# Kernel optimization log

Measured on AMD Instinct MI355X. Metric: run time of the kernel, lower is better.

The kernel has to match this reference:

```python
import jax, jax.numpy as jnp
import numpy as np
from jax import lax
import math

B, T, CIN, H, W = 8, 64, 2, 64, 64
HID, SPK_C = 32, 64
D_MODEL, N_LAYERS, D_STATE, D_CONV = 512, 4, 16, 4
D_INNER = 2 * D_MODEL
DT_RANK = math.ceil(D_MODEL / 16)  # 32
NUM_CLASSES = 11
FEAT = SPK_C * (H // 4) * (W // 4)  # 16384
BETA, THR = 0.9, 1.0

# --- surrogate-gradient spike (snntorch fast_sigmoid, slope=25) ---
@jax.custom_vjp
def spike_fn(x):
    return (x > 0).astype(x.dtype)

def _spike_fwd(x):
    return spike_fn(x), x

def _spike_bwd(x, g):
    return (g / (25.0 * jnp.abs(x) + 1.0) ** 2,)

spike_fn.defvjp(_spike_fwd, _spike_bwd)

def lif(cur, mem):
    # snntorch Leaky, reset_mechanism='subtract': reset from previous mem (detached)
    reset = lax.stop_gradient((mem > THR).astype(mem.dtype))
    mem = BETA * mem + cur - reset * THR
    spk = spike_fn(mem - THR)
    return spk, mem

def conv2d(x, w, b):
    y = lax.conv_general_dilated(x, w, (1, 1), 'SAME', dimension_numbers=('NCHW', 'OIHW', 'NCHW'))
    return y + b[None, :, None, None]

def maxpool2(x):
    return lax.reduce_window(x, -jnp.inf, lax.max, (1, 1, 2, 2), (1, 1, 2, 2), 'VALID')

def layernorm(x, w, b):
    mu = x.mean(-1, keepdims=True)
    var = ((x - mu) ** 2).mean(-1, keepdims=True)
    return (x - mu) * lax.rsqrt(var + 1e-5) * w + b

def frontend(x, c1w, c1b, c2w, c2b, c3w, c3b):
    mem1 = jnp.zeros((B, HID, H // 2, W // 2), x.dtype)
    mem2 = jnp.zeros((B, HID, H // 4, W // 4), x.dtype)
    mem3 = jnp.zeros((B, SPK_C, H // 4, W // 4), x.dtype)
    def step(carry, xt):
        m1, m2, m3 = carry
        s1, m1 = lif(maxpool2(conv2d(xt, c1w, c1b)), m1)
        s2, m2 = lif(maxpool2(conv2d(s1, c2w, c2b)), m2)
        s3, m3 = lif(conv2d(s2, c3w, c3b), m3)
        return (m1, m2, m3), s3
    _, spk = lax.scan(step, (mem1, mem2, mem3), jnp.swapaxes(x, 0, 1))
    return jnp.swapaxes(spk, 0, 1)  # (B,T,SPK_C,H/4,W/4)

def rate_smooth(a):
    # depthwise conv1d over time with kernel ones(5)/5, padding=2 (moving average)
    Tn = a.shape[1]
    ap = jnp.pad(a, ((0, 0), (2, 2), (0, 0)))
    return sum(ap[:, k:k + Tn, :] for k in range(5)) / 5.0

def mamba_block(x, p):
    ln_w, ln_b, in_w, conv_w, xproj_w, dt_w, dt_b, A_log, Dp, out_w = p
    h = layernorm(x, ln_w, ln_b)
    xr = h @ in_w  # (B,L,2*D_INNER)
    xi, res = jnp.split(xr, 2, axis=-1)
    L = xi.shape[1]
    # causal depthwise conv1d (pad D_CONV-1 left, truncate to L)
    xp = jnp.pad(xi, ((0, 0), (D_CONV - 1, 0), (0, 0)))
    xc = sum(conv_w[:, k] * xp[:, k:k + L, :] for k in range(D_CONV))
    xc = jax.nn.silu(xc)
    x_dbl = xc @ xproj_w  # (B,L,DT_RANK+2*D_STATE)
    dt = x_dbl[..., :DT_RANK]
    Bm = x_dbl[..., DT_RANK:DT_RANK + D_STATE]
    Cm = x_dbl[..., DT_RANK + D_STATE:]
    dt = jax.nn.softplus(dt @ dt_w + dt_b)  # (B,L,D_INNER)
    A = -jnp.exp(A_log)  # (D_INNER,D_STATE)
    dA = jnp.exp(dt[..., None] * A)  # (B,L,D_INNER,D_STATE)
    dBu = dt[..., None] * Bm[:, :, None, :] * xc[..., None]
    def step(hst, inp):
        dA_t, dBu_t, C_t = inp
        hst = dA_t * hst + dBu_t
        return hst, jnp.einsum('bdn,bn->bd', hst, C_t)
    h0 = jnp.zeros((x.shape[0], D_INNER, D_STATE), x.dtype)
    _, ys = lax.scan(step, h0, (jnp.swapaxes(dA, 0, 1), jnp.swapaxes(dBu, 0, 1), jnp.swapaxes(Cm, 0, 1)))
    y = jnp.swapaxes(ys, 0, 1) + xc * Dp
    y = y * jax.nn.silu(res)
    return x + y @ out_w

def _forward(x, c1w, c1b, c2w, c2b, c3w, c3b, inp_w, inp_b, ln_w, ln_b, in_w, conv_w, xproj_w, dt_w, dt_b, A_log, Dp, mb_out_w, fn_w, fn_b, cls_w, cls_b):
    spikes = frontend(x, c1w, c1b, c2w, c2b, c3w, c3b)
    act = rate_smooth(spikes.reshape(B, T, -1))
    h = act @ inp_w + inp_b
    def layer(c, p):
        return mamba_block(c, p), None
    h, _ = lax.scan(layer, h, (ln_w, ln_b, in_w, conv_w, xproj_w, dt_w, dt_b, A_log, Dp, mb_out_w))
    h = h.mean(axis=1)
    h = layernorm(h, fn_w, fn_b)
    return h @ cls_w + cls_b

def setup_inputs():
    key = jax.random.key(0)
    ks = jax.random.split(key, 16)
    def gn(k, shape, scale):
        return jax.random.normal(k, shape, jnp.float32) * scale
    x = jax.random.uniform(ks[0], (B, T, CIN, H, W), jnp.float32)
    c1w = gn(ks[1], (HID, CIN, 3, 3), 1.0 / np.sqrt(CIN * 9)); c1b = jnp.zeros((HID,))
    c2w = gn(ks[2], (HID, HID, 3, 3), 1.0 / np.sqrt(HID * 9)); c2b = jnp.zeros((HID,))
    c3w = gn(ks[3], (SPK_C, HID, 3, 3), 1.0 / np.sqrt(HID * 9)); c3b = jnp.zeros((SPK_C,))
    inp_w = gn(ks[4], (FEAT, D_MODEL), 1.0 / np.sqrt(FEAT)); inp_b = jnp.zeros((D_MODEL,))
    ln_w = jnp.ones((N_LAYERS, D_MODEL)); ln_b = jnp.zeros((N_LAYERS, D_MODEL))
    in_w = gn(ks[5], (N_LAYERS, D_MODEL, 2 * D_INNER), 1.0 / np.sqrt(D_MODEL))
    conv_w = gn(ks[6], (N_LAYERS, D_INNER, D_CONV), 1.0 / np.sqrt(D_CONV))
    xproj_w = gn(ks[7], (N_LAYERS, D_INNER, DT_RANK + 2 * D_STATE), 1.0 / np.sqrt(D_INNER))
    dt_w = gn(ks[8], (N_LAYERS, DT_RANK, D_INNER), 1.0 / np.sqrt(DT_RANK))
    dtv = jnp.exp(jax.random.uniform(ks[9], (N_LAYERS, D_INNER)) * (np.log(0.1) - np.log(0.001)) + np.log(0.001))
    dt_b = dtv + jnp.log(-jnp.expm1(-dtv))
    A_log = jnp.log(jnp.broadcast_to(jnp.arange(1, D_STATE + 1, dtype=jnp.float32), (N_LAYERS, D_INNER, D_STATE))) + jnp.zeros((N_LAYERS, D_INNER, D_STATE))
    Dp = jnp.ones((N_LAYERS, D_INNER))
    mb_out_w = gn(ks[10], (N_LAYERS, D_INNER, D_MODEL), 1.0 / np.sqrt(D_INNER))
    fn_w = jnp.ones((D_MODEL,)); fn_b = jnp.zeros((D_MODEL,))
    cls_w = gn(ks[11], (D_MODEL, NUM_CLASSES), 1.0 / np.sqrt(D_MODEL)); cls_b = jnp.zeros((NUM_CLASSES,))
    return dict(x=x, c1w=c1w, c1b=c1b, c2w=c2w, c2b=c2b, c3w=c3w, c3b=c3b, inp_w=inp_w, inp_b=inp_b, ln_w=ln_w, ln_b=ln_b, in_w=in_w, conv_w=conv_w, xproj_w=xproj_w, dt_w=dt_w, dt_b=dt_b, A_log=A_log, Dp=Dp, mb_out_w=mb_out_w, fn_w=fn_w, fn_b=fn_b, cls_w=cls_w, cls_b=cls_b)

def reference(x, c1w, c1b, c2w, c2b, c3w, c3b, inp_w, inp_b, ln_w, ln_b, in_w, conv_w, xproj_w, dt_w, dt_b, A_log, Dp, mb_out_w, fn_w, fn_b, cls_w, cls_b):
    return _forward(x, c1w, c1b, c2w, c2b, c3w, c3b, inp_w, inp_b, ln_w, ln_b, in_w, conv_w, xproj_w, dt_w, dt_b, A_log, Dp, mb_out_w, fn_w, fn_b, cls_w, cls_b)
```

## Files before the change

kernel.cpp:

```cpp
#include <hip/hip_runtime.h>
#include <math.h>


static constexpr int TT = 64;
static constexpr float BETA = 0.9f, THR = 1.0f;


__global__ __launch_bounds__(256) void k_conv1pool(const float* __restrict__ x,
    const float* __restrict__ w, const float* __restrict__ bias, float* __restrict__ out)
{
    __shared__ float sI[2 * 66 * 76];
    __shared__ float sW[576];
    const int bt = blockIdx.x;
    const int tid = threadIdx.x;
    for (int i = tid; i < 2 * 66 * 76; i += 256) sI[i] = 0.f;
    for (int i = tid; i < 576; i += 256) sW[i] = w[i];
    __syncthreads();
    const float* img = x + (size_t)bt * 8192;
    for (int i = tid; i < 2048; i += 256) {
        float4 v4 = ((const float4*)img)[i];
        int lin = i * 4;
        int ci = lin >> 12, rc = lin & 4095;
        int r = rc >> 6, c = rc & 63;
        *(float4*)&sI[ci * 5016 + (r + 1) * 76 + (c + 4)] = v4;
    }
    __syncthreads();
    const int oh = tid >> 3;
    const int p8 = (tid & 7) * 8;
    float v[2][4][10];
    #pragma unroll
    for (int ci = 0; ci < 2; ++ci) {
        #pragma unroll
        for (int dr = 0; dr < 4; ++dr) {
            const float* rp = &sI[ci * 5016 + (2 * oh + dr) * 76 + p8];
            float2 a  = *(const float2*)&rp[2];
            float4 b4 = *(const float4*)&rp[4];
            float4 c4 = *(const float4*)&rp[8];
            float2 e  = *(const float2*)&rp[12];
            v[ci][dr][0] = a.y;
            v[ci][dr][1] = b4.x; v[ci][dr][2] = b4.y; v[ci][dr][3] = b4.z; v[ci][dr][4] = b4.w;
            v[ci][dr][5] = c4.x; v[ci][dr][6] = c4.y; v[ci][dr][7] = c4.z; v[ci][dr][8] = c4.w;
            v[ci][dr][9] = e.x;
        }
    }
    const int ow0 = (tid & 7) * 4;
    float* obase = out + (size_t)bt * 32768;
    for (int co = 0; co < 32; ++co) {
        float pos[2][8];
        #pragma unroll
        for (int i = 0; i < 2; ++i)
            #pragma unroll
            for (int j = 0; j < 8; ++j) pos[i][j] = 0.f;
        #pragma unroll
        for (int ci = 0; ci < 2; ++ci) {
            const float* wp = &sW[(co * 2 + ci) * 9];
            float w0=wp[0],w1=wp[1],w2=wp[2],w3=wp[3],w4=wp[4],w5=wp[5],w6=wp[6],w7=wp[7],w8=wp[8];
            #pragma unroll
            for (int pr = 0; pr < 2; ++pr)
                #pragma unroll
                for (int pc = 0; pc < 8; ++pc)
                    pos[pr][pc] += v[ci][pr][pc]*w0 + v[ci][pr][pc+1]*w1 + v[ci][pr][pc+2]*w2
                                 + v[ci][pr+1][pc]*w3 + v[ci][pr+1][pc+1]*w4 + v[ci][pr+1][pc+2]*w5
                                 + v[ci][pr+2][pc]*w6 + v[ci][pr+2][pc+1]*w7 + v[ci][pr+2][pc+2]*w8;
        }
        float b0 = bias[co];
        float4 o;
        o.x = fmaxf(fmaxf(pos[0][0], pos[0][1]), fmaxf(pos[1][0], pos[1][1])) + b0;
        o.y = fmaxf(fmaxf(pos[0][2], pos[0][3]), fmaxf(pos[1][2], pos[1][3])) + b0;
        o.z = fmaxf(fmaxf(pos[0][4], pos[0][5]), fmaxf(pos[1][4], pos[1][5])) + b0;
        o.w = fmaxf(fmaxf(pos[0][6], pos[0][7]), fmaxf(pos[1][6], pos[1][7])) + b0;
        *(float4*)&obase[co * 1024 + oh * 32 + ow0] = o;
    }
}

__global__ __launch_bounds__(256) void k_lif(const float* __restrict__ cur,
                                             float* __restrict__ spk, int chw)
{
    int idx = blockIdx.x * 256 + threadIdx.x;
    int b = idx / chw, p = idx % chw;
    const float* cp = cur + (size_t)b * TT * chw + p;
    float* sp = spk + (size_t)b * TT * chw + p;
    float m = 0.f;
    for (int t = 0; t < TT; ++t) {
        float c = cp[(size_t)t * chw];
        float reset = (m > THR) ? THR : 0.f;
        m = BETA * m + c - reset;
        sp[(size_t)t * chw] = (m > THR) ? 1.f : 0.f;
    }
}

__global__ __launch_bounds__(256) void k_conv2(const float* __restrict__ s1,
    const float* __restrict__ w, const float* __restrict__ bias, float* __restrict__ out)
{
    __shared__ float sI[4 * 34 * 40];
    __shared__ float sW2[4 * 8 * 12];
    const int bt = blockIdx.x;
    const int co0 = blockIdx.y * 8;
    const int tid = threadIdx.x;
    for (int i = tid; i < 4 * 34 * 40; i += 256) sI[i] = 0.f;
    const int cc = tid & 31;
    const int g8 = ((tid >> 5) & 3) * 8;
    const int cq = (tid >> 7) * 4;
    float acc[4][8] = {};
    const float* img = s1 + (size_t)bt * 32768;
    for (int chunk = 0; chunk < 8; ++chunk) {
        __syncthreads();
        const float* src = img + chunk * 4096;
        for (int i = tid; i < 1024; i += 256) {
            float4 v4 = ((const float4*)src)[i];
            int lin = i * 4;
            int ci = lin >> 10, rc = lin & 1023;
            int r = rc >> 5, c = rc & 31;
            *(float4*)&sI[ci * 1360 + (r + 1) * 40 + (c + 4)] = v4;
        }
        for (int i = tid; i < 4 * 8 * 9; i += 256) {
            int ci4 = i / 72, rest = i % 72;
            int co = rest / 9, k = rest % 9;
            sW2[(ci4 * 8 + co) * 12 + k] = w[((co0 + co) * 32 + chunk * 4 + ci4) * 9 + k];
        }
        __syncthreads();
        #pragma unroll
        for (int ci4 = 0; ci4 < 4; ++ci4) {
            float win[10][3];
            #pragma unroll
            for (int dr = 0; dr < 10; ++dr) {
                const float* sp = &sI[ci4 * 1360 + (g8 + dr) * 40 + cc + 3];
                win[dr][0] = sp[0]; win[dr][1] = sp[1]; win[dr][2] = sp[2];
            }
            #pragma unroll
            for (int co = 0; co < 4; ++co) {
                const float4* wq = (const float4*)&sW2[(ci4 * 8 + cq + co) * 12];
                float4 wa = wq[0], wb = wq[1], wc = wq[2];
                #pragma unroll
                for (int p = 0; p < 8; ++p)
                    acc[co][p] += win[p][0]*wa.x + win[p][1]*wa.y + win[p][2]*wa.z
                                + win[p+1][0]*wa.w + win[p+1][1]*wb.x + win[p+1][2]*wb.y
                                + win[p+2][0]*wb.z + win[p+2][1]*wb.w + win[p+2][2]*wc.x;
            }
        }
    }
    const bool writer = (cc & 1) == 0;
    #pragma unroll
    for (int co = 0; co < 4; ++co) {
        float b0 = bias[co0 + cq + co];
        float* ob = out + (size_t)bt * 8192 + (co0 + cq + co) * 256;
        #pragma unroll
        for (int i = 0; i < 4; ++i) {
            float v = fmaxf(acc[co][2 * i], acc[co][2 * i + 1]);
            v = fmaxf(v, __shfl_xor(v, 1, 64));
            if (writer) ob[(g8 / 2 + i) * 16 + (cc >> 1)] = v + b0;
        }
    }
}

__global__ __launch_bounds__(256) void k_conv3(const float* __restrict__ s2,
    const float* __restrict__ w, const float* __restrict__ bias, float* __restrict__ out)
{
    __shared__ float sI[8 * 18 * 24];
    __shared__ float sW3[8 * 32 * 12];
    const int bt = blockIdx.x;
    const int co0 = blockIdx.y * 32;
    const int tid = threadIdx.x;
    for (int i = tid; i < 8 * 18 * 24; i += 256) sI[i] = 0.f;
    const int cc = tid & 15;
    const int g8 = ((tid >> 4) & 1) * 8;
    const int cq = (tid >> 5) * 4;
    float acc[4][8] = {};
    const float* img = s2 + (size_t)bt * 8192;
    for (int chunk = 0; chunk < 4; ++chunk) {
        __syncthreads();
        const float* src = img + chunk * 2048;
        for (int i = tid; i < 512; i += 256) {
            float4 v4 = ((const float4*)src)[i];
            int lin = i * 4;
            int ci = lin >> 8, rc = lin & 255;
            int r = rc >> 4, c = rc & 15;
            *(float4*)&sI[ci * 432 + (r + 1) * 24 + (c + 4)] = v4;
        }
        for (int i = tid; i < 8 * 32 * 9; i += 256) {
            int ci = i / 288, rest = i % 288;
            int co = rest / 9, k = rest % 9;
            sW3[(ci * 32 + co) * 12 + k] = w[((co0 + co) * 32 + chunk * 8 + ci) * 9 + k];
        }
        __syncthreads();
        #pragma unroll
        for (int ci = 0; ci < 8; ++ci) {
            float win[10][3];
            #pragma unroll
            for (int dr = 0; dr < 10; ++dr) {
                const float* sp = &sI[ci * 432 + (g8 + dr) * 24 + cc + 3];
                win[dr][0] = sp[0]; win[dr][1] = sp[1]; win[dr][2] = sp[2];
            }
            #pragma unroll
            for (int co = 0; co < 4; ++co) {
                const float4* wq = (const float4*)&sW3[(ci * 32 + cq + co) * 12];
                float4 wa = wq[0], wb = wq[1], wc = wq[2];
                #pragma unroll
                for (int p = 0; p < 8; ++p)
                    acc[co][p] += win[p][0]*wa.x + win[p][1]*wa.y + win[p][2]*wa.z
                                + win[p+1][0]*wa.w + win[p+1][1]*wb.x + win[p+1][2]*wb.y
                                + win[p+2][0]*wb.z + win[p+2][1]*wb.w + win[p+2][2]*wc.x;
            }
        }
    }
    #pragma unroll
    for (int co = 0; co < 4; ++co) {
        float b0 = bias[co0 + cq + co];
        float* ob = out + (size_t)bt * 16384 + (co0 + cq + co) * 256;
        #pragma unroll
        for (int p = 0; p < 8; ++p)
            ob[(g8 + p) * 16 + cc] = acc[co][p] + b0;
    }
}

__global__ __launch_bounds__(256) void k_lif3smooth(const float* __restrict__ cur,
                                                    float* __restrict__ act)
{
    int idx = blockIdx.x * 256 + threadIdx.x;
    int b = idx >> 14, f = idx & 16383;
    const float* cp = cur + (size_t)b * TT * 16384 + f;
    float* ap = act + (size_t)b * TT * 16384 + f;
    float m = 0.f;
    float s0 = 0, s1 = 0, s2 = 0, s3 = 0, s4 = 0;
    for (int t = 0; t < TT + 2; ++t) {
        float s = 0.f;
        if (t < TT) {
            float cv = cp[(size_t)t * 16384];
            float reset = (m > THR) ? THR : 0.f;
            m = BETA * m + cv - reset;
            s = (m > THR) ? 1.f : 0.f;
        }
        s4 = s3; s3 = s2; s2 = s1; s1 = s0; s0 = s;
        if (t >= 2) ap[(size_t)(t - 2) * 16384] = (s0 + s1 + s2 + s3 + s4) * 0.2f;
    }
}


__global__ __launch_bounds__(256) void k_gemm(const float* __restrict__ A,
    const float* __restrict__ Bm, float* __restrict__ C, int M, int N, int K)
{
    __shared__ float As[16][68];
    __shared__ float Bs[16][68];
    const int tid = threadIdx.x;
    const int n0 = blockIdx.x * 64, m0 = blockIdx.y * 64;
    const int kchunk = K / gridDim.z;
    const int k0 = blockIdx.z * kchunk, k1 = k0 + kchunk;
    const int ar = tid >> 2, ac = (tid & 3) * 4;
    const int br = tid >> 4, bc = (tid & 15) * 4;
    const int row0 = (tid >> 4) * 4, col0 = (tid & 15) * 4;
    float acc[4][4] = {};
    float4 av = *(const float4*)&A[(size_t)(m0 + ar) * K + k0 + ac];
    float4 bv = *(const float4*)&Bm[(size_t)(k0 + br) * N + n0 + bc];
    for (int kk = k0; kk < k1; kk += 16) {
        As[ac + 0][ar] = av.x; As[ac + 1][ar] = av.y;
        As[ac + 2][ar] = av.z; As[ac + 3][ar] = av.w;
        *(float4*)&Bs[br][bc] = bv;
        __syncthreads();
        if (kk + 16 < k1) {
            av = *(const float4*)&A[(size_t)(m0 + ar) * K + kk + 16 + ac];
            bv = *(const float4*)&Bm[(size_t)(kk + 16 + br) * N + n0 + bc];
        }
        #pragma unroll
        for (int k = 0; k < 16; ++k) {
            float4 a4 = *(const float4*)&As[k][row0];
            float4 b4 = *(const float4*)&Bs[k][col0];
            acc[0][0] += a4.x * b4.x; acc[0][1] += a4.x * b4.y; acc[0][2] += a4.x * b4.z; acc[0][3] += a4.x * b4.w;
            acc[1][0] += a4.y * b4.x; acc[1][1] += a4.y * b4.y; acc[1][2] += a4.y * b4.z; acc[1][3] += a4.y * b4.w;
            acc[2][0] += a4.z * b4.x; acc[2][1] += a4.z * b4.y; acc[2][2] += a4.z * b4.z; acc[2][3] += a4.z * b4.w;
            acc[3][0] += a4.w * b4.x; acc[3][1] += a4.w * b4.y; acc[3][2] += a4.w * b4.z; acc[3][3] += a4.w * b4.w;
        }
        __syncthreads();
    }
    float* Cp = C + (size_t)blockIdx.z * M * N;
    #pragma unroll
    for (int i = 0; i < 4; ++i) {
        float4 o;
        o.x = acc[i][0]; o.y = acc[i][1]; o.z = acc[i][2]; o.w = acc[i][3];
        *(float4*)&Cp[(size_t)(m0 + row0 + i) * N + n0 + col0] = o;
    }
}

template <bool ADD, bool BIAS>
__global__ __launch_bounds__(256) void k_reduce(const float* __restrict__ part,
    const float* __restrict__ bias, float* __restrict__ out, int MN, int N, int KS)
{
    int i4 = (blockIdx.x * 256 + threadIdx.x) * 4;
    if (i4 >= MN) return;
    float4 v = {0.f, 0.f, 0.f, 0.f};
    for (int z = 0; z < KS; ++z) {
        float4 p = *(const float4*)&part[(size_t)z * MN + i4];
        v.x += p.x; v.y += p.y; v.z += p.z; v.w += p.w;
    }
    if (BIAS) {
        float4 bv = *(const float4*)&bias[i4 % N];
        v.x += bv.x; v.y += bv.y; v.z += bv.z; v.w += bv.w;
    }
    if (ADD) {
        float4 o = *(const float4*)&out[i4];
        v.x += o.x; v.y += o.y; v.z += o.z; v.w += o.w;
    }
    *(float4*)&out[i4] = v;
}


__device__ __forceinline__ float blockSum(float v, float* red)
{
    #pragma unroll
    for (int o = 32; o; o >>= 1) v += __shfl_down(v, o, 64);
    const int wv = threadIdx.x >> 6, lane = threadIdx.x & 63;
    if (lane == 0) red[wv] = v;
    __syncthreads();
    float r = red[0] + red[1] + red[2] + red[3];
    __syncthreads();
    return r;
}

__global__ __launch_bounds__(256) void k_ln(const float* __restrict__ x,
    const float* __restrict__ w, const float* __restrict__ b, float* __restrict__ out)
{
    __shared__ float red[4];
    int row = blockIdx.x;
    const float* xp = x + (size_t)row * 512;
    int c = threadIdx.x * 2;
    float2 v = *(const float2*)&xp[c];
    float mu = blockSum(v.x + v.y, red) * (1.f / 512.f);
    float d0 = v.x - mu, d1 = v.y - mu;
    float var = blockSum(d0 * d0 + d1 * d1, red) * (1.f / 512.f);
    float inv = rsqrtf(var + 1e-5f);
    float2 o;
    o.x = d0 * inv * w[c] + b[c];
    o.y = d1 * inv * w[c + 1] + b[c + 1];
    *(float2*)&out[(size_t)row * 512 + c] = o;
}

__global__ __launch_bounds__(256) void k_convsilu(const float* __restrict__ xr,
    const float* __restrict__ cw, float* __restrict__ xc)
{
    int idx = blockIdx.x * 256 + threadIdx.x;
    int row = idx >> 10;
    int d = idx & 1023;
    int t = row & 63;
    const float* xi = xr + (size_t)(row - t) * 2048 + d;
    float4 w = *(const float4*)&cw[d * 4];
    float a = w.w * xi[(size_t)t * 2048];
    if (t >= 1) a += w.z * xi[(size_t)(t - 1) * 2048];
    if (t >= 2) a += w.y * xi[(size_t)(t - 2) * 2048];
    if (t >= 3) a += w.x * xi[(size_t)(t - 3) * 2048];
    xc[idx] = a / (1.f + __expf(-a));
}

__global__ __launch_bounds__(256) void k_xproj(const float* __restrict__ xc,
    const float* __restrict__ w, float* __restrict__ xdbl)
{
    int row = blockIdx.x * 4 + (threadIdx.x >> 6);
    int col = threadIdx.x & 63;
    const float* a = xc + (size_t)row * 1024;
    float acc = 0.f;
    #pragma unroll 4
    for (int k = 0; k < 1024; k += 4) {
        float4 av = *(const float4*)&a[k];
        acc += av.x * w[(size_t)k * 64 + col] + av.y * w[(size_t)(k + 1) * 64 + col]
             + av.z * w[(size_t)(k + 2) * 64 + col] + av.w * w[(size_t)(k + 3) * 64 + col];
    }
    xdbl[(size_t)row * 64 + col] = acc;
}

__global__ __launch_bounds__(256) void k_dtproj(const float* __restrict__ xdbl,
    const float* __restrict__ w, const float* __restrict__ bias, float* __restrict__ dt)
{
    int idx = blockIdx.x * 256 + threadIdx.x;
    int row = idx >> 10, d = idx & 1023;
    const float* a = xdbl + (size_t)row * 64;
    float acc = bias[d];
    #pragma unroll 8
    for (int r = 0; r < 32; ++r) acc += a[r] * w[(size_t)r * 1024 + d];
    dt[idx] = fmaxf(acc, 0.f) + log1pf(__expf(-fabsf(acc)));
}

__global__ __launch_bounds__(256) void k_scan(const float* __restrict__ dt,
    const float* __restrict__ xc, const float* __restrict__ xdbl,
    const float* __restrict__ xr, const float* __restrict__ A_log,
    const float* __restrict__ Dp, float* __restrict__ y)
{
    const int tid = threadIdx.x;
    const int lane = tid & 63;
    const int half = lane >> 5;
    const int p = blockIdx.x * 128 + (tid >> 6) * 32 + (lane & 31);
    const int b = p >> 10, d = p & 1023;
    float A[8];
    #pragma unroll
    for (int n = 0; n < 8; ++n) A[n] = -__expf(A_log[d * 16 + half * 8 + n]);
    float Dv = Dp[d];
    float h[8] = {};
    const int row0 = b * 64;
    size_t base = (size_t)row0 * 1024 + d;
    float dtv = dt[base], xv = xc[base];
    float res = xr[(size_t)row0 * 2048 + 1024 + d];
    const float4* Bp = (const float4*)&xdbl[(size_t)row0 * 64 + 32 + half * 8];
    const float4* Cq = (const float4*)&xdbl[(size_t)row0 * 64 + 48 + half * 8];
    float4 B0 = Bp[0], B1 = Bp[1];
    float4 C0 = Cq[0], C1 = Cq[1];
    for (int t = 0; t < TT; ++t) {
        float dtv_n = 0.f, xv_n = 0.f, res_n = 0.f;
        float4 B0n = {}, B1n = {}, C0n = {}, C1n = {};
        if (t < TT - 1) {
            size_t b2 = base + (size_t)(t + 1) * 1024;
            dtv_n = dt[b2]; xv_n = xc[b2];
            res_n = xr[(size_t)(row0 + t + 1) * 2048 + 1024 + d];
            const float4* Bp2 = (const float4*)&xdbl[(size_t)(row0 + t + 1) * 64 + 32 + half * 8];
            const float4* Cq2 = (const float4*)&xdbl[(size_t)(row0 + t + 1) * 64 + 48 + half * 8];
            B0n = Bp2[0]; B1n = Bp2[1]; C0n = Cq2[0]; C1n = Cq2[1];
        }
        float dtx = dtv * xv;
        float acch = 0.f;
        #define SCAN_STEP(Bv, Cv, n0)                                             \
        {                                                                         \
            float bb[4] = {Bv.x, Bv.y, Bv.z, Bv.w};                               \
            float cv[4] = {Cv.x, Cv.y, Cv.z, Cv.w};                               \
            _Pragma("unroll")                                                     \
            for (int r = 0; r < 4; ++r) {                                         \
                int n = n0 + r;                                                   \
                float hv = __expf(dtv * A[n]) * h[n] + dtx * bb[r];               \
                h[n] = hv;                                                        \
                acch += hv * cv[r];                                               \
            }                                                                     \
        }
        SCAN_STEP(B0, C0, 0) SCAN_STEP(B1, C1, 4)
        #undef SCAN_STEP
        float acc = acch + __shfl_xor(acch, 32, 64);
        float sil = res / (1.f + __expf(-res));
        if (half == 0)
            y[(size_t)(row0 + t) * 1024 + d] = (acc + xv * Dv) * sil;
        dtv = dtv_n; xv = xv_n; res = res_n;
        B0 = B0n; B1 = B1n; C0 = C0n; C1 = C1n;
    }
}

__global__ __launch_bounds__(256) void k_meant(const float* __restrict__ h,
                                               float* __restrict__ hm)
{
    int idx = blockIdx.x * 256 + threadIdx.x;
    int b = idx >> 9, d = idx & 511;
    const float* p = h + (size_t)b * 64 * 512 + d;
    float s = 0.f;
    for (int t = 0; t < 64; ++t) s += p[t * 512];
    hm[idx] = s * (1.f / 64.f);
}

__global__ __launch_bounds__(256) void k_final(const float* __restrict__ hm,
    const float* __restrict__ fw, const float* __restrict__ fb,
    const float* __restrict__ cw, const float* __restrict__ cb, float* __restrict__ out)
{
    __shared__ float red[4];
    __shared__ float nrm[512];
    int b = blockIdx.x;
    const float* xp = hm + (size_t)b * 512;
    int c2 = threadIdx.x * 2;
    float2 v = *(const float2*)&xp[c2];
    float mu = blockSum(v.x + v.y, red) * (1.f / 512.f);
    float d0 = v.x - mu, d1 = v.y - mu;
    float var = blockSum(d0 * d0 + d1 * d1, red) * (1.f / 512.f);
    float inv = rsqrtf(var + 1e-5f);
    nrm[c2] = d0 * inv * fw[c2] + fb[c2];
    nrm[c2 + 1] = d1 * inv * fw[c2 + 1] + fb[c2 + 1];
    __syncthreads();
    for (int c = 0; c < 11; ++c) {
        float p = nrm[threadIdx.x] * cw[threadIdx.x * 11 + c]
                + nrm[threadIdx.x + 256] * cw[(threadIdx.x + 256) * 11 + c];
        float s = blockSum(p, red);
        if (threadIdx.x == 0) out[b * 11 + c] = s + cb[c];
    }
}


extern "C" void kernel_launch(void* const* d_in, const int* in_sizes, int n_in,
                              void* d_out, int out_size, void* d_ws, size_t ws_size,
                              hipStream_t stream)
{
    const float* x      = (const float*)d_in[0];
    const float* c1w    = (const float*)d_in[1];
    const float* c1b    = (const float*)d_in[2];
    const float* c2w    = (const float*)d_in[3];
    const float* c2b    = (const float*)d_in[4];
    const float* c3w    = (const float*)d_in[5];
    const float* c3b    = (const float*)d_in[6];
    const float* inp_w  = (const float*)d_in[7];
    const float* inp_b  = (const float*)d_in[8];
    const float* ln_w   = (const float*)d_in[9];
    const float* ln_b   = (const float*)d_in[10];
    const float* in_w   = (const float*)d_in[11];
    const float* conv_w = (const float*)d_in[12];
    const float* xproj_w= (const float*)d_in[13];
    const float* dt_w   = (const float*)d_in[14];
    const float* dt_b   = (const float*)d_in[15];
    const float* A_log  = (const float*)d_in[16];
    const float* Dp     = (const float*)d_in[17];
    const float* mb_out_w=(const float*)d_in[18];
    const float* fn_w   = (const float*)d_in[19];
    const float* fn_b   = (const float*)d_in[20];
    const float* cls_w  = (const float*)d_in[21];
    const float* cls_b  = (const float*)d_in[22];
    float* out = (float*)d_out;

    float* ws   = (float*)d_ws;
    float* bufA = ws;
    float* bufB = bufA + 16777216;
    float* h    = bufB + 16777216;
    float* hn   = h    + 262144;
    float* xr   = hn   + 262144;
    float* xc   = xr   + 1048576;
    float* xdbl = xc   + 524288;
    float* dtb  = xdbl + 32768;
    float* yb   = dtb  + 524288;
    float* hm   = yb   + 524288;

    k_conv1pool<<<512, 256, 0, stream>>>(x, c1w, c1b, bufA);
    k_lif<<<1024, 256, 0, stream>>>(bufA, bufB, 32768);
    k_conv2<<<dim3(512, 4), 256, 0, stream>>>(bufB, c2w, c2b, bufA);
    k_lif<<<256, 256, 0, stream>>>(bufA, bufB, 8192);
    k_conv3<<<dim3(512, 2), 256, 0, stream>>>(bufB, c3w, c3b, bufA);
    k_lif3smooth<<<512, 256, 0, stream>>>(bufA, bufB);

    k_gemm<<<dim3(8, 8, 32), 256, 0, stream>>>(bufB, inp_w, bufA, 512, 512, 16384);
    k_reduce<false, true><<<256, 256, 0, stream>>>(bufA, inp_b, h, 262144, 512, 32);

    for (int l = 0; l < 4; ++l) {
        k_ln<<<512, 256, 0, stream>>>(h, ln_w + l * 512, ln_b + l * 512, hn);
        k_gemm<<<dim3(32, 8, 8), 256, 0, stream>>>(hn, in_w + (size_t)l * 1048576, bufA, 512, 2048, 512);
        k_reduce<false, false><<<1024, 256, 0, stream>>>(bufA, nullptr, xr, 1048576, 2048, 8);
        k_convsilu<<<2048, 256, 0, stream>>>(xr, conv_w + l * 4096, xc);
        k_xproj<<<128, 256, 0, stream>>>(xc, xproj_w + l * 65536, xdbl);
        k_dtproj<<<2048, 256, 0, stream>>>(xdbl, dt_w + l * 32768, dt_b + l * 1024, dtb);
        k_scan<<<64, 256, 0, stream>>>(dtb, xc, xdbl, xr, A_log + l * 16384, Dp + l * 1024, yb);
        k_gemm<<<dim3(8, 8, 16), 256, 0, stream>>>(yb, mb_out_w + (size_t)l * 524288, bufA, 512, 512, 1024);
        k_reduce<true, false><<<256, 256, 0, stream>>>(bufA, nullptr, h, 262144, 512, 16);
    }

    k_meant<<<16, 256, 0, stream>>>(h, hm);
    k_final<<<8, 256, 0, stream>>>(hm, fn_w, fn_b, cls_w, cls_b, out);
}
```

Before: 1.112 ms.

## Prefetch conv2/conv3 stages into registers, halve channel tiles, retune scan and split-K

conv2 and conv3 now load the next input chunk and its weights into registers while the current chunk is computed, then write them to shared memory, overlapping global loads with math. Each block handles half as many output channels, doubling the grid for more parallelism at the cost of re-reading the input tile. The scan kernel moves to 64-thread blocks across 256 blocks to spread work over more CUs. Split-K factors for the in_proj and out_proj GEMMs are halved to cut partial-sum traffic in the reduce kernels.

```diff
diff --git a/kernel.cpp b/kernel.cpp
--- a/kernel.cpp
+++ b/kernel.cpp
@@ -93,31 +93,45 @@
     const float* __restrict__ w, const float* __restrict__ bias, float* __restrict__ out)
 {
     __shared__ float sI[4 * 34 * 40];
-    __shared__ float sW2[4 * 8 * 12];
+    __shared__ float sW2[4 * 4 * 12];
     const int bt = blockIdx.x;
-    const int co0 = blockIdx.y * 8;
+    const int co0 = blockIdx.y * 4;
     const int tid = threadIdx.x;
     for (int i = tid; i < 4 * 34 * 40; i += 256) sI[i] = 0.f;
     const int cc = tid & 31;
     const int g8 = ((tid >> 5) & 3) * 8;
-    const int cq = (tid >> 7) * 4;
-    float acc[4][8] = {};
+    const int cq = (tid >> 7) * 2;
+    float acc[2][8] = {};
     const float* img = s1 + (size_t)bt * 32768;
-    for (int chunk = 0; chunk < 8; ++chunk) {
-        __syncthreads();
-        const float* src = img + chunk * 4096;
-        for (int i = tid; i < 1024; i += 256) {
-            float4 v4 = ((const float4*)src)[i];
-            int lin = i * 4;
+
+    const int wci = tid / 36, wrest = tid % 36;
+    const int wco = wrest / 9, wk = wrest % 9;
+    const bool wok = tid < 144;
+
+    float4 pf0, pf1, pf2, pf3;
+    float pw = 0.f;
+    auto loadStage = [&](int chunk) {
+        const float4* src = (const float4*)(img + chunk * 4096);
+        pf0 = src[tid]; pf1 = src[tid + 256]; pf2 = src[tid + 512]; pf3 = src[tid + 768];
+        if (wok) pw = w[((co0 + wco) * 32 + chunk * 4 + wci) * 9 + wk];
+    };
+    auto writeStage = [&]() {
+        #pragma unroll
+        for (int j = 0; j < 4; ++j) {
+            float4 v4 = (j == 0) ? pf0 : (j == 1) ? pf1 : (j == 2) ? pf2 : pf3;
+            int lin = (tid + j * 256) * 4;
             int ci = lin >> 10, rc = lin & 1023;
             int r = rc >> 5, c = rc & 31;
             *(float4*)&sI[ci * 1360 + (r + 1) * 40 + (c + 4)] = v4;
         }
-        for (int i = tid; i < 4 * 8 * 9; i += 256) {
-            int ci4 = i / 72, rest = i % 72;
-            int co = rest / 9, k = rest % 9;
-            sW2[(ci4 * 8 + co) * 12 + k] = w[((co0 + co) * 32 + chunk * 4 + ci4) * 9 + k];
-        }
+        if (wok) sW2[(wci * 4 + wco) * 12 + wk] = pw;
+    };
+
+    loadStage(0);
+    __syncthreads();
+    for (int chunk = 0; chunk < 8; ++chunk) {
+        writeStage();
+        if (chunk < 7) loadStage(chunk + 1);
         __syncthreads();
         #pragma unroll
         for (int ci4 = 0; ci4 < 4; ++ci4) {
@@ -128,8 +142,8 @@
                 win[dr][0] = sp[0]; win[dr][1] = sp[1]; win[dr][2] = sp[2];
             }
             #pragma unroll
-            for (int co = 0; co < 4; ++co) {
-                const float4* wq = (const float4*)&sW2[(ci4 * 8 + cq + co) * 12];
+            for (int co = 0; co < 2; ++co) {
+                const float4* wq = (const float4*)&sW2[(ci4 * 4 + cq + co) * 12];
                 float4 wa = wq[0], wb = wq[1], wc = wq[2];
                 #pragma unroll
                 for (int p = 0; p < 8; ++p)
@@ -138,10 +152,11 @@
                                 + win[p+2][0]*wb.z + win[p+2][1]*wb.w + win[p+2][2]*wc.x;
             }
         }
+        __syncthreads();
     }
     const bool writer = (cc & 1) == 0;
     #pragma unroll
-    for (int co = 0; co < 4; ++co) {
+    for (int co = 0; co < 2; ++co) {
         float b0 = bias[co0 + cq + co];
         float* ob = out + (size_t)bt * 8192 + (co0 + cq + co) * 256;
         #pragma unroll
@@ -157,31 +172,57 @@
     const float* __restrict__ w, const float* __restrict__ bias, float* __restrict__ out)
 {
     __shared__ float sI[8 * 18 * 24];
-    __shared__ float sW3[8 * 32 * 12];
+    __shared__ float sW3[8 * 16 * 12];
     const int bt = blockIdx.x;
-    const int co0 = blockIdx.y * 32;
+    const int co0 = blockIdx.y * 16;
     const int tid = threadIdx.x;
     for (int i = tid; i < 8 * 18 * 24; i += 256) sI[i] = 0.f;
     const int cc = tid & 15;
     const int g8 = ((tid >> 4) & 1) * 8;
-    const int cq = (tid >> 5) * 4;
-    float acc[4][8] = {};
+    const int cq = (tid >> 5) * 2;
+    float acc[2][8] = {};
     const float* img = s2 + (size_t)bt * 8192;
-    for (int chunk = 0; chunk < 4; ++chunk) {
-        __syncthreads();
-        const float* src = img + chunk * 2048;
-        for (int i = tid; i < 512; i += 256) {
-            float4 v4 = ((const float4*)src)[i];
-            int lin = i * 4;
+
+    float4 pf0, pf1;
+    float pw[5];
+    auto loadStage = [&](int chunk) {
+        const float4* src = (const float4*)(img + chunk * 2048);
+        pf0 = src[tid]; pf1 = src[tid + 256];
+        #pragma unroll
+        for (int j = 0; j < 5; ++j) {
+            int i = tid + j * 256;
+            if (i < 1152) {
+                int ci = i / 144, rest = i % 144;
+                int co = rest / 9, k = rest % 9;
+                pw[j] = w[((co0 + co) * 32 + chunk * 8 + ci) * 9 + k];
+            }
+        }
+    };
+    auto writeStage = [&]() {
+        #pragma unroll
+        for (int j = 0; j < 2; ++j) {
+            float4 v4 = (j == 0) ? pf0 : pf1;
+            int lin = (tid + j * 256) * 4;
             int ci = lin >> 8, rc = lin & 255;
             int r = rc >> 4, c = rc & 15;
             *(float4*)&sI[ci * 432 + (r + 1) * 24 + (c + 4)] = v4;
         }
-        for (int i = tid; i < 8 * 32 * 9; i += 256) {
-            int ci = i / 288, rest = i % 288;
-            int co = rest / 9, k = rest % 9;
-            sW3[(ci * 32 + co) * 12 + k] = w[((co0 + co) * 32 + chunk * 8 + ci) * 9 + k];
-        }
+        #pragma unroll
+        for (int j = 0; j < 5; ++j) {
+            int i = tid + j * 256;
+            if (i < 1152) {
+                int ci = i / 144, rest = i % 144;
+                int co = rest / 9, k = rest % 9;
+                sW3[(ci * 16 + co) * 12 + k] = pw[j];
+            }
+        }
+    };
+
+    loadStage(0);
+    __syncthreads();
+    for (int chunk = 0; chunk < 4; ++chunk) {
+        writeStage();
+        if (chunk < 3) loadStage(chunk + 1);
         __syncthreads();
         #pragma unroll
         for (int ci = 0; ci < 8; ++ci) {
@@ -192,8 +233,8 @@
                 win[dr][0] = sp[0]; win[dr][1] = sp[1]; win[dr][2] = sp[2];
             }
             #pragma unroll
-            for (int co = 0; co < 4; ++co) {
-                const float4* wq = (const float4*)&sW3[(ci * 32 + cq + co) * 12];
+            for (int co = 0; co < 2; ++co) {
+                const float4* wq = (const float4*)&sW3[(ci * 16 + cq + co) * 12];
                 float4 wa = wq[0], wb = wq[1], wc = wq[2];
                 #pragma unroll
                 for (int p = 0; p < 8; ++p)
@@ -202,9 +243,10 @@
                                 + win[p+2][0]*wb.z + win[p+2][1]*wb.w + win[p+2][2]*wc.x;
             }
         }
+        __syncthreads();
     }
     #pragma unroll
-    for (int co = 0; co < 4; ++co) {
+    for (int co = 0; co < 2; ++co) {
         float b0 = bias[co0 + cq + co];
         float* ob = out + (size_t)bt * 16384 + (co0 + cq + co) * 256;
         #pragma unroll
@@ -377,15 +419,14 @@
     dt[idx] = fmaxf(acc, 0.f) + log1pf(__expf(-fabsf(acc)));
 }
 
-__global__ __launch_bounds__(256) void k_scan(const float* __restrict__ dt,
+__global__ __launch_bounds__(64) void k_scan(const float* __restrict__ dt,
     const float* __restrict__ xc, const float* __restrict__ xdbl,
     const float* __restrict__ xr, const float* __restrict__ A_log,
     const float* __restrict__ Dp, float* __restrict__ y)
 {
-    const int tid = threadIdx.x;
-    const int lane = tid & 63;
+    const int lane = threadIdx.x & 63;
     const int half = lane >> 5;
-    const int p = blockIdx.x * 128 + (tid >> 6) * 32 + (lane & 31);
+    const int p = blockIdx.x * 32 + (lane & 31);
     const int b = p >> 10, d = p & 1023;
     float A[8];
     #pragma unroll
@@ -516,9 +557,9 @@
 
     k_conv1pool<<<512, 256, 0, stream>>>(x, c1w, c1b, bufA);
     k_lif<<<1024, 256, 0, stream>>>(bufA, bufB, 32768);
-    k_conv2<<<dim3(512, 4), 256, 0, stream>>>(bufB, c2w, c2b, bufA);
+    k_conv2<<<dim3(512, 8), 256, 0, stream>>>(bufB, c2w, c2b, bufA);
     k_lif<<<256, 256, 0, stream>>>(bufA, bufB, 8192);
-    k_conv3<<<dim3(512, 2), 256, 0, stream>>>(bufB, c3w, c3b, bufA);
+    k_conv3<<<dim3(512, 4), 256, 0, stream>>>(bufB, c3w, c3b, bufA);
     k_lif3smooth<<<512, 256, 0, stream>>>(bufA, bufB);
 
     k_gemm<<<dim3(8, 8, 32), 256, 0, stream>>>(bufB, inp_w, bufA, 512, 512, 16384);
@@ -526,14 +567,14 @@
 
     for (int l = 0; l < 4; ++l) {
         k_ln<<<512, 256, 0, stream>>>(h, ln_w + l * 512, ln_b + l * 512, hn);
-        k_gemm<<<dim3(32, 8, 8), 256, 0, stream>>>(hn, in_w + (size_t)l * 1048576, bufA, 512, 2048, 512);
-        k_reduce<false, false><<<1024, 256, 0, stream>>>(bufA, nullptr, xr, 1048576, 2048, 8);
+        k_gemm<<<dim3(32, 8, 4), 256, 0, stream>>>(hn, in_w + (size_t)l * 1048576, bufA, 512, 2048, 512);
+        k_reduce<false, false><<<1024, 256, 0, stream>>>(bufA, nullptr, xr, 1048576, 2048, 4);
         k_convsilu<<<2048, 256, 0, stream>>>(xr, conv_w + l * 4096, xc);
         k_xproj<<<128, 256, 0, stream>>>(xc, xproj_w + l * 65536, xdbl);
         k_dtproj<<<2048, 256, 0, stream>>>(xdbl, dt_w + l * 32768, dt_b + l * 1024, dtb);
-        k_scan<<<64, 256, 0, stream>>>(dtb, xc, xdbl, xr, A_log + l * 16384, Dp + l * 1024, yb);
-        k_gemm<<<dim3(8, 8, 16), 256, 0, stream>>>(yb, mb_out_w + (size_t)l * 524288, bufA, 512, 512, 1024);
-        k_reduce<true, false><<<256, 256, 0, stream>>>(bufA, nullptr, h, 262144, 512, 16);
+        k_scan<<<256, 64, 0, stream>>>(dtb, xc, xdbl, xr, A_log + l * 16384, Dp + l * 1024, yb);
+        k_gemm<<<dim3(8, 8, 8), 256, 0, stream>>>(yb, mb_out_w + (size_t)l * 524288, bufA, 512, 512, 1024);
+        k_reduce<true, false><<<256, 256, 0, stream>>>(bufA, nullptr, h, 262144, 512, 8);
     }
 
     k_meant<<<16, 256, 0, stream>>>(h, hm);
```

Result: no change. 1.100 ms (-1.0%).
